# Optimization experiments

Measured on AMD Instinct MI355X. Metric: run time of the kernel, lower is better.

The kernel has to match this reference:

```python
import jax, jax.numpy as jnp
import numpy as np

B, I, O, ORDER = 16384, 256, 256, 8
LO, HI = -1.0, 1.0


def setup_inputs() -> dict:
    key = jax.random.key(0)
    k1, k2, k3 = jax.random.split(key, 3)
    x = jax.random.normal(k1, (B, I), dtype=jnp.float32)
    weights = jax.random.normal(k2, (O, I), dtype=jnp.float32)
    # BernsteinBasisFunction init: randn(order+1) * 0.1, one per (o, i) pair
    coeffs = jax.random.normal(k3, (O, I, ORDER + 1), dtype=jnp.float32) * 0.1
    return {"x": x, "weights": weights, "coeffs": coeffs}


def reference(x, weights, coeffs):
    # x: [B, I]; weights: [O, I]; coeffs: [O, I, K+1]
    K = coeffs.shape[-1] - 1
    zoom = (HI - LO) / 2.0
    pan = (HI + LO) / 2.0
    xt = jnp.tanh(x) * zoom + pan          # squash into [LO, HI]
    x_a = xt - LO                          # [B, I]
    x_b = HI - xt                          # [B, I]
    e = jnp.arange(K + 1)
    # ber[b, i, k] = x_a^k * x_b^(K-k)  (unnormalized Bernstein basis)
    ber = (x_a[..., None] ** e) * (x_b[..., None] ** (K - e))  # [B, I, K+1]
    # transformed[b, o, i] = sum_k coeffs[o,i,k] * ber[b,i,k]; out = einsum('boi,oi->bo')
    # Fused: fold weights into coeffs to avoid the [B, O, I] intermediate.
    wc = coeffs * weights[..., None]       # [O, I, K+1]
    return jnp.einsum('bik,oik->bo', ber, wc)
```

## Files before the change

### kernel.cpp

```cpp
#include <hip/hip_runtime.h>
#include <hip/hip_bf16.h>


#define BDIM 16384
#define IDIM 256
#define ODIM 256
#define NK 9
#define NSTEP 36
#define STEP_ELEMS (ODIM * 64)
#define GSTEP 3
#define NGROUP 12

typedef short short8 __attribute__((ext_vector_type(8)));
typedef float floatx4 __attribute__((ext_vector_type(4)));

__global__ __launch_bounds__(256) void prep_wc3(const float* __restrict__ weights,
                                                const float* __restrict__ coeffs,
                                                ushort* __restrict__ wc) {
    __shared__ float cl[IDIM * NK];
    const int o = blockIdx.x;
    const int t = threadIdx.x;
    const float* cb = coeffs + (size_t)o * (IDIM * NK);
#pragma unroll
    for (int j = 0; j < NK; ++j)
        cl[t + 256 * j] = cb[t + 256 * j];
    __syncthreads();

    const float wv = weights[o * IDIM + t];
    const int ic = t >> 6, il = t & 63;
    const int s = il >> 5, quad = (il >> 3) & 3, j = il & 7;
    const size_t base = (size_t)((((o >> 4) * 2 + s) * 64) + (o & 15) + quad * 16) * 8 + j;
    ushort* wb = wc + base;
#pragma unroll
    for (int k = 0; k < NK; ++k) {
        __hip_bfloat16 b = __float2bfloat16(cl[t * NK + k] * wv);
        wb[(size_t)(ic * NK + k) * STEP_ELEMS] = *(ushort*)&b;
    }
}

__global__ __launch_bounds__(256, 3) void bern_gemm(const float* __restrict__ x,
                                                    const ushort* __restrict__ wc,
                                                    float* __restrict__ out) {
    __shared__ ushort Blds[2][GSTEP * 4096];

    const int tid  = threadIdx.x;
    const int wave = tid >> 6;
    const int lane = tid & 63;
    const int cg   = blockIdx.x & 3;
    const int rb   = (blockIdx.x >> 2) * 128 + wave * 32;
    const int lrow = lane & 15;
    const int jseg = (lane >> 4) * 8;

    float p[2][2][8];
    float r[2][2][8];
    float xb[2][2][8];
    floatx4 acc[2][4];
    floatx4 zero = {0.0f, 0.0f, 0.0f, 0.0f};
#pragma unroll
    for (int m = 0; m < 2; ++m)
#pragma unroll
        for (int n = 0; n < 4; ++n)
            acc[m][n] = zero;

#define LOAD_X(ic_)                                                             \
    {                                                                           \
        _Pragma("unroll") for (int m = 0; m < 2; ++m)                           \
        _Pragma("unroll") for (int s = 0; s < 2; ++s) {                         \
            const float* xp = x + (size_t)(rb + m * 16 + lrow) * IDIM           \
                              + (ic_) * 64 + s * 32 + jseg;                     \
            float4 v0 = *(const float4*)(xp);                                   \
            float4 v1 = *(const float4*)(xp + 4);                               \
            xb[m][s][0] = v0.x; xb[m][s][1] = v0.y;                             \
            xb[m][s][2] = v0.z; xb[m][s][3] = v0.w;                             \
            xb[m][s][4] = v1.x; xb[m][s][5] = v1.y;                             \
            xb[m][s][6] = v1.z; xb[m][s][7] = v1.w;                             \
        }                                                                       \
    }

#define SETUP_BASIS()                                                           \
    {                                                                           \
        _Pragma("unroll") for (int m = 0; m < 2; ++m)                           \
        _Pragma("unroll") for (int s = 0; s < 2; ++s)                           \
        _Pragma("unroll") for (int e = 0; e < 8; ++e) {                         \
            float t  = __builtin_amdgcn_exp2f(xb[m][s][e] * 2.8853900817779268f);\
            float q  = 2.0f * __builtin_amdgcn_rcpf(t + 1.0f);                  \
            float q2 = q * q;                                                   \
            float q4 = q2 * q2;                                                 \
            p[m][s][e] = q4 * q4;                                               \
            r[m][s][e] = t;                                                     \
        }                                                                       \
    }

#define STAGE(g_, b_)                                                           \
    {                                                                           \
        _Pragma("unroll") for (int q = 0; q < GSTEP; ++q)                       \
        _Pragma("unroll") for (int h = 0; h < 2; ++h) {                         \
            int st  = (g_) * GSTEP + q;                                         \
            const ushort* sp = wc + (size_t)st * STEP_ELEMS + cg * 4096         \
                               + h * 2048 + wave * 512 + lane * 8;              \
            ushort* dp = &Blds[b_][q * 4096 + h * 2048 + wave * 512 + lane * 8];\
            __builtin_amdgcn_global_load_lds(                                   \
                (const __attribute__((address_space(1))) void*)sp,              \
                (__attribute__((address_space(3))) void*)dp, 16, 0, 0);         \
        }                                                                       \
    }

    LOAD_X(0);
    STAGE(0, 0);

#pragma unroll 1
    for (int g = 0; g < NGROUP; ++g) {
        __syncthreads();
        if (g + 1 < NGROUP) STAGE(g + 1, (g + 1) & 1);

        const int ic = g / 3;
        const int gm = g - ic * 3;
        if (gm == 0) SETUP_BASIS();
        if (gm == 1 && ic + 1 < 4) LOAD_X(ic + 1);

        const ushort* Bp = Blds[g & 1];
#pragma unroll
        for (int q = 0; q < GSTEP; ++q) {
            const int kc = gm * 3 + q;
            short8 bfr[2][4];
#pragma unroll
            for (int s = 0; s < 2; ++s)
#pragma unroll
                for (int n = 0; n < 4; ++n)
                    bfr[s][n] = *(const short8*)&Bp[q * 4096 + (n * 2 + s) * 512 + lane * 8];

#pragma unroll
            for (int s = 0; s < 2; ++s)
#pragma unroll
                for (int m = 0; m < 2; ++m) {
                    union { short8 v; __hip_bfloat162 h2[4]; } pk;
#pragma unroll
                    for (int e = 0; e < 8; e += 2)
                        pk.h2[e >> 1] = __float22bfloat162_rn(
                            make_float2(p[m][s][e], p[m][s][e + 1]));
#pragma unroll
                    for (int n = 0; n < 4; ++n)
                        acc[m][n] = __builtin_amdgcn_mfma_f32_16x16x32_bf16(
                            pk.v, bfr[s][n], acc[m][n], 0, 0, 0);
                    if (kc < NK - 1)
#pragma unroll
                        for (int e = 0; e < 8; ++e) p[m][s][e] *= r[m][s][e];
                }
        }
    }

#pragma unroll
    for (int m = 0; m < 2; ++m) {
#pragma unroll
        for (int n = 0; n < 4; ++n) {
            int col   = cg * 64 + n * 16 + (lane & 15);
            int rbase = rb + m * 16 + (lane >> 4) * 4;
#pragma unroll
            for (int reg = 0; reg < 4; ++reg) {
                out[(size_t)(rbase + reg) * ODIM + col] = acc[m][n][reg];
            }
        }
    }
#undef LOAD_X
#undef SETUP_BASIS
#undef STAGE
}

extern "C" void kernel_launch(void* const* d_in, const int* in_sizes, int n_in,
                              void* d_out, int out_size, void* d_ws, size_t ws_size,
                              hipStream_t stream) {
    const float* x       = (const float*)d_in[0];
    const float* weights = (const float*)d_in[1];
    const float* coeffs  = (const float*)d_in[2];
    float* out = (float*)d_out;
    ushort* wc = (ushort*)d_ws;

    prep_wc3<<<ODIM, 256, 0, stream>>>(weights, coeffs, wc);
    bern_gemm<<<512, 256, 0, stream>>>(x, wc, out);
}
```

Measured before the change: 112.3 us.

## Split K reduction across two wave halves within each block and reduce via LDS

Each block now runs 512 threads: two groups of four waves each process half of the 36 K-steps (two input-column chunks each) for the same 128x64 output tile. Partial accumulators are combined through LDS at the end. The aim is to double the waves per block, giving more latency hiding and a shorter serial K loop, since the grid of 512 blocks cannot supply more parallelism. The cost is an extra LDS reduction, extra barriers, a larger LDS footprint per block, and higher register pressure under the 512-thread launch bound.

```diff
diff --git a/kernel.cpp b/kernel.cpp
--- a/kernel.cpp
+++ b/kernel.cpp
@@ -6,10 +6,9 @@
 #define IDIM 256
 #define ODIM 256
 #define NK 9
-#define NSTEP 36
 #define STEP_ELEMS (ODIM * 64)
-#define GSTEP 3
-#define NGROUP 12
+#define GSTEP 2
+#define NGROUP 9
 
 typedef short short8 __attribute__((ext_vector_type(8)));
 typedef float floatx4 __attribute__((ext_vector_type(4)));
@@ -38,18 +37,21 @@
     }
 }
 
-__global__ __launch_bounds__(256, 3) void bern_gemm(const float* __restrict__ x,
+__global__ __launch_bounds__(512, 4) void bern_gemm(const float* __restrict__ x,
                                                     const ushort* __restrict__ wc,
                                                     float* __restrict__ out) {
-    __shared__ ushort Blds[2][GSTEP * 4096];
+    __shared__ ushort stage[2][2][GSTEP * 4096];
 
     const int tid  = threadIdx.x;
     const int wave = tid >> 6;
     const int lane = tid & 63;
+    const int half = wave >> 2;
+    const int w4   = wave & 3;
     const int cg   = blockIdx.x & 3;
-    const int rb   = (blockIdx.x >> 2) * 128 + wave * 32;
+    const int rb   = (blockIdx.x >> 2) * 128 + w4 * 32;
     const int lrow = lane & 15;
     const int jseg = (lane >> 4) * 8;
+    const int kbase = half * 18;
 
     float p[2][2][8];
     float r[2][2][8];
@@ -94,34 +96,34 @@
 #define STAGE(g_, b_)                                                           \
     {                                                                           \
         _Pragma("unroll") for (int q = 0; q < GSTEP; ++q)                       \
-        _Pragma("unroll") for (int h = 0; h < 2; ++h) {                         \
-            int st  = (g_) * GSTEP + q;                                         \
-            const ushort* sp = wc + (size_t)st * STEP_ELEMS + cg * 4096         \
-                               + h * 2048 + wave * 512 + lane * 8;              \
-            ushort* dp = &Blds[b_][q * 4096 + h * 2048 + wave * 512 + lane * 8];\
+        _Pragma("unroll") for (int d = 0; d < 2; ++d) {                         \
+            int st = kbase + (g_) * GSTEP + q;                                  \
+            int off = w4 * 1024 + d * 512 + lane * 8;                           \
+            const ushort* sp = wc + (size_t)st * STEP_ELEMS + cg * 4096 + off;  \
+            ushort* dp = &stage[half][b_][q * 4096 + off];                      \
             __builtin_amdgcn_global_load_lds(                                   \
                 (const __attribute__((address_space(1))) void*)sp,              \
                 (__attribute__((address_space(3))) void*)dp, 16, 0, 0);         \
         }                                                                       \
     }
 
-    LOAD_X(0);
+    LOAD_X(2 * half);
+    SETUP_BASIS();
     STAGE(0, 0);
 
 #pragma unroll 1
     for (int g = 0; g < NGROUP; ++g) {
         __syncthreads();
         if (g + 1 < NGROUP) STAGE(g + 1, (g + 1) & 1);
+        if (g == 2) LOAD_X(2 * half + 1);
 
-        const int ic = g / 3;
-        const int gm = g - ic * 3;
-        if (gm == 0) SETUP_BASIS();
-        if (gm == 1 && ic + 1 < 4) LOAD_X(ic + 1);
-
-        const ushort* Bp = Blds[g & 1];
+        const ushort* Bp = stage[half][g & 1];
 #pragma unroll
         for (int q = 0; q < GSTEP; ++q) {
-            const int kc = gm * 3 + q;
+            const int t = g * GSTEP + q;
+            if (t == 9) SETUP_BASIS();
+            const int kc = (t >= 9) ? (t - 9) : t;
+
             short8 bfr[2][4];
 #pragma unroll
             for (int s = 0; s < 2; ++s)
@@ -149,17 +151,33 @@
         }
     }
 
+    __syncthreads();
+    float* red = (float*)&stage[0][0][0];
+    if (half == 1) {
 #pragma unroll
-    for (int m = 0; m < 2; ++m) {
+        for (int m = 0; m < 2; ++m)
 #pragma unroll
-        for (int n = 0; n < 4; ++n) {
-            int col   = cg * 64 + n * 16 + (lane & 15);
-            int rbase = rb + m * 16 + (lane >> 4) * 4;
+            for (int n = 0; n < 4; ++n) {
+                int col = n * 16 + (lane & 15);
+                int rl  = w4 * 32 + m * 16 + (lane >> 4) * 4;
 #pragma unroll
-            for (int reg = 0; reg < 4; ++reg) {
-                out[(size_t)(rbase + reg) * ODIM + col] = acc[m][n][reg];
+                for (int reg = 0; reg < 4; ++reg)
+                    red[(rl + reg) * 65 + col] = acc[m][n][reg];
             }
-        }
+    }
+    __syncthreads();
+    if (half == 0) {
+#pragma unroll
+        for (int m = 0; m < 2; ++m)
+#pragma unroll
+            for (int n = 0; n < 4; ++n) {
+                int col = n * 16 + (lane & 15);
+                int rl  = w4 * 32 + m * 16 + (lane >> 4) * 4;
+#pragma unroll
+                for (int reg = 0; reg < 4; ++reg)
+                    out[(size_t)(rb + m * 16 + (lane >> 4) * 4 + reg) * ODIM
+                        + cg * 64 + col] = acc[m][n][reg] + red[(rl + reg) * 65 + col];
+            }
     }
 #undef LOAD_X
 #undef SETUP_BASIS
@@ -176,5 +194,5 @@
     ushort* wc = (ushort*)d_ws;
 
     prep_wc3<<<ODIM, 256, 0, stream>>>(weights, coeffs, wc);
-    bern_gemm<<<512, 256, 0, stream>>>(x, wc, out);
+    bern_gemm<<<512, 512, 0, stream>>>(x, wc, out);
 }
```

Measured after the change: 146.6 us. 1.31x slower.
